# Optimization experiments

Hardware: AMD Instinct MI355X
Metric: run time of the kernel (lower is better)

## Reference

```python
import jax, jax.numpy as jnp
import numpy as np

# pywt 'db4' decomposition low-pass filter (orthogonal Daubechies-4, 8 taps)
_DB4_DEC_LO = np.array([
    -0.010597401784997278, 0.032883011666982945,
     0.030841381835986965, -0.18703481171888114,
    -0.02798376941698385,  0.6308807679295904,
     0.7148465705525415,   0.23037781330885523], dtype=np.float32)
_REC_LO = _DB4_DEC_LO[::-1].copy()                                   # reconstruction low-pass
_REC_HI = (_DB4_DEC_LO * ((-1.0) ** np.arange(8))).astype(np.float32)  # reconstruction high-pass
LEVEL = 3


def _iswt_level(lo, hi, w, dilation):
    """One inverse-SWT level: periodic a-trous synthesis, halved tight-frame dual.
    lo, hi: (BN, T); w: (1, 2, Lf) correlation kernel (rec filters pre-flipped)."""
    Lf = w.shape[-1]
    padl, padr = dilation * (Lf // 2), dilation * (Lf // 2 - 1)
    x = jnp.stack([lo, hi], axis=1)  # (BN, 2, T)
    x = jnp.pad(x, ((0, 0), (0, 0), (padl, padr)), mode="wrap")  # periodic boundary
    y = jax.lax.conv_general_dilated(
        x, w, window_strides=(1,), padding="VALID",
        rhs_dilation=(dilation,),
        dimension_numbers=("NCH", "OIH", "NCH"))  # (BN, 1, T)
    return 0.5 * y[:, 0, :]


def _iswt(coeffs):
    """coeffs: (B, N, T, level+1) with last dim ordered [cA_n, cD_n, ..., cD_1].
    Faithfully mirrors the torch module: it builds the list [cD_1,...,cD_n,cA_n]
    and hands it to ptwt.iswt, which treats element 0 as the running approximation
    and iterates the remaining bands with dilation 2**(n_details - pos - 1)."""
    B, N, T, nb = coeffs.shape
    c = coeffs.reshape(B * N, T, nb)
    w = jnp.stack([jnp.asarray(_REC_LO)[::-1],
                   jnp.asarray(_REC_HI)[::-1]])[None].astype(coeffs.dtype)  # (1,2,Lf)
    order = list(range(nb - 1, 0, -1)) + [0]  # [cD_1, ..., cD_n, cA_n]
    res_lo = c[:, :, order[0]]
    details = order[1:]
    for pos, idx in enumerate(details):
        dilation = 2 ** (len(details) - pos - 1)
        res_lo = _iswt_level(res_lo, c[:, :, idx], w, dilation)
    return res_lo.reshape(B, N, T)


def setup_inputs() -> dict:
    key = jax.random.key(0)
    coeffs = jax.random.normal(key, (32, 128, 4096, LEVEL + 1), dtype=jnp.float32)
    return {"coeffs": coeffs}


def reference(coeffs):
    return _iswt(coeffs)
```

## Files before the change

### kernel.cpp

```cpp
#include <hip/hip_runtime.h>

static constexpr float H0 = -0.010597401784997278f;
static constexpr float H1 =  0.032883011666982945f;
static constexpr float H2 =  0.030841381835986965f;
static constexpr float H3 = -0.18703481171888114f;
static constexpr float H4 = -0.02798376941698385f;
static constexpr float H5 =  0.6308807679295904f;
static constexpr float H6 =  0.7148465705525415f;
static constexpr float H7 =  0.23037781330885523f;

static constexpr float W0[8] = { 0.5f*H0,  0.5f*H1,  0.5f*H2,  0.5f*H3,
                                 0.5f*H4,  0.5f*H5,  0.5f*H6,  0.5f*H7 };
static constexpr float W1[8] = {-0.5f*H7,  0.5f*H6, -0.5f*H5,  0.5f*H4,
                                -0.5f*H3,  0.5f*H2, -0.5f*H1,  0.5f*H0 };

constexpr int T     = 4096;
constexpr int BANDF = 1216;

static __device__ __forceinline__ int paddr_g(int g) { return (g << 2) + ((g >> 3) << 2); }
static __device__ __forceinline__ int paddr_f(int f) { return f + ((f >> 5) << 2); }

template <int D, int NG>
static __device__ __forceinline__ void level_acc(const float* __restrict__ lo,
                                                 const float* __restrict__ hi,
                                                 int lg, float acc[4])
{
    acc[0] = acc[1] = acc[2] = acc[3] = 0.0f;
#pragma unroll
    for (int j = 0; j < NG; ++j) {
        const int a = paddr_g(lg - D + j);
        const float4 vl = *(const float4*)(lo + a);
        const float4 vh = *(const float4*)(hi + a);
        const float l[4] = {vl.x, vl.y, vl.z, vl.w};
        const float h[4] = {vh.x, vh.y, vh.z, vh.w};
#pragma unroll
        for (int m = 0; m < 4; ++m) {
            const int w = 4 * j + m;
#pragma unroll
            for (int jp = 0; jp < 4; ++jp) {
                const int d = w - jp;
                if (d >= 0 && (d % D) == 0 && (d / D) < 8) {
                    const int k = d / D;
                    acc[jp] = fmaf(W0[k], l[m], acc[jp]);
                    acc[jp] = fmaf(W1[k], h[m], acc[jp]);
                }
            }
        }
    }
}

__global__ __launch_bounds__(256, 6)
void iswt_kernel(const float* __restrict__ in, float* __restrict__ out)
{
    __shared__ __align__(16) float X[BANDF], Y[BANDF], Z[BANDF];

    const int t   = threadIdx.x;
    const int bid = blockIdx.x;
    const int row = bid >> 2;
    const int t0  = (bid & 3) << 10;

    const float4* __restrict__ src = (const float4*)(in + (size_t)row * (T * 4));

    float hA[5], hD3[5];
#pragma unroll
    for (int j = 0; j < 4; ++j) {
        const int fp = t + (j << 8);
        const int P  = (t0 - 28 + fp) & (T - 1);
        const float4 v = src[P];
        const int a = paddr_f(fp);
        X[a] = v.w;  Y[a] = v.z;
        hA[j] = v.x; hD3[j] = v.y;
    }
    if (t < 52) {
        const int fp = 1024 + t;
        const int P  = (t0 - 28 + fp) & (T - 1);
        const float4 v = src[P];
        const int a = paddr_f(fp);
        X[a] = v.w;  Y[a] = v.z;
        hA[4] = v.x; hD3[4] = v.y;
    }
    __syncthreads();

    {
        float r[4];
        level_acc<4, 8>(X, Y, 4 + t, r);
        *(float4*)(Z + paddr_g(4 + t)) = make_float4(r[0], r[1], r[2], r[3]);
        if (t < 6) {
            float rt[4];
            level_acc<4, 8>(X, Y, 260 + t, rt);
            *(float4*)(Z + paddr_g(260 + t)) = make_float4(rt[0], rt[1], rt[2], rt[3]);
        }
    }
    __syncthreads();

#pragma unroll
    for (int j = 0; j < 4; ++j) {
        const int a = paddr_f(t + (j << 8));
        X[a] = hD3[j];  Y[a] = hA[j];
    }
    if (t < 52) {
        const int a = paddr_f(1024 + t);
        X[a] = hD3[4];  Y[a] = hA[4];
    }
    __syncthreads();

    float r2[4], r2t[4];
    level_acc<2, 5>(Z, X, 6 + t, r2);
    if (t < 2) level_acc<2, 5>(Z, X, 262 + t, r2t);
    __syncthreads();

    *(float4*)(X + paddr_g(6 + t)) = make_float4(r2[0], r2[1], r2[2], r2[3]);
    if (t < 2) *(float4*)(X + paddr_g(262 + t)) = make_float4(r2t[0], r2t[1], r2t[2], r2t[3]);
    __syncthreads();

    float r3[4];
    level_acc<1, 3>(X, Y, 7 + t, r3);
    *(float4*)(out + (size_t)row * T + t0 + (t << 2)) =
        make_float4(r3[0], r3[1], r3[2], r3[3]);
}

extern "C" void kernel_launch(void* const* d_in, const int* in_sizes, int n_in,
                              void* d_out, int out_size, void* d_ws, size_t ws_size,
                              hipStream_t stream)
{
    const float* coeffs = (const float*)d_in[0];
    float* out = (float*)d_out;
    const int nrows = in_sizes[0] / (T * 4);
    iswt_kernel<<<nrows * 4, 256, 0, stream>>>(coeffs, out);
}
```

Baseline: 73.01 us.

## Stage input via direct global-to-LDS loads and deinterleave all bands in shared memory

Replaces the per-thread float4 global loads with __builtin_amdgcn_global_load_lds into a staging buffer, then deinterleaves all four bands into separate shared arrays at once. Because all bands stay in LDS, the register-held bands and the second store pass are gone, along with one barrier. The staging buffer and one band array are reused as scratch for the level outputs. Shared memory per block grows to about 37 KB, so the occupancy hint drops from 6 to 4 blocks, and the extra LDS round-trip may cost more than the register traffic it removes.

```diff
diff --git a/kernel.cpp b/kernel.cpp
--- a/kernel.cpp
+++ b/kernel.cpp
@@ -15,7 +15,8 @@
                                 -0.5f*H3,  0.5f*H2, -0.5f*H1,  0.5f*H0 };
 
 constexpr int T     = 4096;
-constexpr int BANDF = 1216;
+constexpr int IPOS  = 1088;
+constexpr int BANDF = 1220;
 
 static __device__ __forceinline__ int paddr_g(int g) { return (g << 2) + ((g >> 3) << 2); }
 static __device__ __forceinline__ int paddr_f(int f) { return f + ((f >> 5) << 2); }
@@ -49,72 +50,71 @@
     }
 }
 
-__global__ __launch_bounds__(256, 6)
+__global__ __launch_bounds__(256, 4)
 void iswt_kernel(const float* __restrict__ in, float* __restrict__ out)
 {
-    __shared__ __align__(16) float X[BANDF], Y[BANDF], Z[BANDF];
+    __shared__ __align__(16) float I[IPOS * 4];
+    __shared__ __align__(16) float A[BANDF], B[BANDF], C[BANDF], Dd[BANDF];
 
-    const int t   = threadIdx.x;
-    const int bid = blockIdx.x;
-    const int row = bid >> 2;
-    const int t0  = (bid & 3) << 10;
+    const int t    = threadIdx.x;
+    const int bid  = blockIdx.x;
+    const int row  = bid >> 2;
+    const int t0   = (bid & 3) << 10;
+    const int lane = t & 63;
+    const int wv   = t >> 6;
 
     const float4* __restrict__ src = (const float4*)(in + (size_t)row * (T * 4));
 
-    float hA[5], hD3[5];
+    for (int c = wv; c < 17; c += 4) {
+        const int pp = (t0 - 28 + (c << 6) + lane) & (T - 1);
+        __builtin_amdgcn_global_load_lds(
+            (const __attribute__((address_space(1))) void*)(src + pp),
+            (__attribute__((address_space(3))) void*)(I + (c << 8)),
+            16, 0, 0);
+    }
+    __syncthreads();
+
 #pragma unroll
     for (int j = 0; j < 4; ++j) {
-        const int fp = t + (j << 8);
-        const int P  = (t0 - 28 + fp) & (T - 1);
-        const float4 v = src[P];
-        const int a = paddr_f(fp);
-        X[a] = v.w;  Y[a] = v.z;
-        hA[j] = v.x; hD3[j] = v.y;
+        const int p = t + (j << 8);
+        const float4 v = *(const float4*)(I + (p << 2));
+        const int a = paddr_f(p);
+        A[a] = v.x;  B[a] = v.y;  C[a] = v.z;  Dd[a] = v.w;
     }
-    if (t < 52) {
-        const int fp = 1024 + t;
-        const int P  = (t0 - 28 + fp) & (T - 1);
-        const float4 v = src[P];
-        const int a = paddr_f(fp);
-        X[a] = v.w;  Y[a] = v.z;
-        hA[4] = v.x; hD3[4] = v.y;
+    if (t < 64) {
+        const int p = 1024 + t;
+        const float4 v = *(const float4*)(I + (p << 2));
+        const int a = paddr_f(p);
+        A[a] = v.x;  B[a] = v.y;  C[a] = v.z;  Dd[a] = v.w;
     }
     __syncthreads();
 
     {
         float r[4];
-        level_acc<4, 8>(X, Y, 4 + t, r);
-        *(float4*)(Z + paddr_g(4 + t)) = make_float4(r[0], r[1], r[2], r[3]);
+        level_acc<4, 8>(Dd, C, 4 + t, r);
+        *(float4*)(I + paddr_g(4 + t)) = make_float4(r[0], r[1], r[2], r[3]);
         if (t < 6) {
             float rt[4];
-            level_acc<4, 8>(X, Y, 260 + t, rt);
-            *(float4*)(Z + paddr_g(260 + t)) = make_float4(rt[0], rt[1], rt[2], rt[3]);
+            level_acc<4, 8>(Dd, C, 260 + t, rt);
+            *(float4*)(I + paddr_g(260 + t)) = make_float4(rt[0], rt[1], rt[2], rt[3]);
         }
     }
     __syncthreads();
 
-#pragma unroll
-    for (int j = 0; j < 4; ++j) {
-        const int a = paddr_f(t + (j << 8));
-        X[a] = hD3[j];  Y[a] = hA[j];
-    }
-    if (t < 52) {
-        const int a = paddr_f(1024 + t);
-        X[a] = hD3[4];  Y[a] = hA[4];
+    {
+        float r[4];
+        level_acc<2, 5>(I, B, 6 + t, r);
+        *(float4*)(Dd + paddr_g(6 + t)) = make_float4(r[0], r[1], r[2], r[3]);
+        if (t < 2) {
+            float rt[4];
+            level_acc<2, 5>(I, B, 262 + t, rt);
+            *(float4*)(Dd + paddr_g(262 + t)) = make_float4(rt[0], rt[1], rt[2], rt[3]);
+        }
     }
     __syncthreads();
 
-    float r2[4], r2t[4];
-    level_acc<2, 5>(Z, X, 6 + t, r2);
-    if (t < 2) level_acc<2, 5>(Z, X, 262 + t, r2t);
-    __syncthreads();
-
-    *(float4*)(X + paddr_g(6 + t)) = make_float4(r2[0], r2[1], r2[2], r2[3]);
-    if (t < 2) *(float4*)(X + paddr_g(262 + t)) = make_float4(r2t[0], r2t[1], r2t[2], r2t[3]);
-    __syncthreads();
-
     float r3[4];
-    level_acc<1, 3>(X, Y, 7 + t, r3);
+    level_acc<1, 3>(Dd, A, 7 + t, r3);
     *(float4*)(out + (size_t)row * T + t0 + (t << 2)) =
         make_float4(r3[0], r3[1], r3[2], r3[3]);
 }
```

Measured after the change: 74.01 us. About the same (+1.4%).
